# Kernel optimization log

Hardware: AMD Instinct MI355X
Metric: run time of the kernel (lower is better)

## Reference

```python
import jax, jax.numpy as jnp
import numpy as np

B, S, F, U = 64, 512, 128, 512          # seq_length == units (required for broadcast in original code)
SIGDIM = F + F * F                       # level-2 truncated signature dimension
GRID_SIZE, SPLINE_ORDER = 5, 3           # efficient-KAN style defaults
NB = GRID_SIZE + SPLINE_ORDER            # number of b-spline basis functions per input feature
LN_EPS = 1e-3                            # keras LayerNormalization default epsilon


def _make_grid():
    h = 2.0 / GRID_SIZE  # uniform grid on [-1, 1], extended by spline order
    return -1.0 + h * jnp.arange(-SPLINE_ORDER, GRID_SIZE + SPLINE_ORDER + 1, dtype=jnp.float32)


def _b_splines(x, grid):
    # x: (N, F) -> (N, F, NB) via Cox-de Boor recursion
    x = x[..., None]
    bases = ((x >= grid[:-1]) & (x < grid[1:])).astype(x.dtype)
    for p in range(1, SPLINE_ORDER + 1):
        left = (x - grid[:-(p + 1)]) / (grid[p:-1] - grid[:-(p + 1)])
        right = (grid[p + 1:] - x) / (grid[p + 1:] - grid[1:-p])
        bases = left * bases[..., :-1] + right * bases[..., 1:]
    return bases


def _kan_linear(x, base_w, spline_w, grid):
    # KANLinear, no bias / no layernorm: silu base branch + b-spline branch
    lead = x.shape[:-1]
    base = jax.nn.silu(x) @ base_w                                  # (..., U)
    b = _b_splines(x.reshape(-1, x.shape[-1]), grid)                # (N, F, NB)
    spl = jnp.einsum('nfk,ufk->nu', b, spline_w).reshape(*lead, base_w.shape[1])
    return base + spl


def _signature2(x):
    # level-2 path signature of piecewise-linear path x: (B, S, F) -> (B, F + F*F)
    dx = x[:, 1:] - x[:, :-1]                                       # (B, S-1, F)
    s1 = dx.sum(axis=1)                                             # (B, F)
    cs = jnp.cumsum(dx, axis=1)
    prev = jnp.concatenate([jnp.zeros_like(cs[:, :1]), cs[:, :-1]], axis=1)
    s2 = jnp.einsum('bti,btj->bij', prev + 0.5 * dx, dx)            # (B, F, F)
    return jnp.concatenate([s1, s2.reshape(x.shape[0], -1)], axis=-1)


def _grkan(sig, w1, b1, w2, b2, w3, b3, w4, b4, ws, bs, gamma, beta):
    # gated residual network mapping signature -> softmax attention weights (B, U)
    h = jax.nn.elu(sig @ w1 + b1)
    h = h @ w2 + b2
    glu = jax.nn.sigmoid(h @ w3 + b3) * (h @ w4 + b4)
    y = sig @ ws + bs + glu
    mu = jnp.mean(y, axis=-1, keepdims=True)
    var = jnp.var(y, axis=-1, keepdims=True)
    y = (y - mu) / jnp.sqrt(var + LN_EPS) * gamma + beta
    return jax.nn.softmax(y, axis=-1)


def setup_inputs() -> dict:
    key = jax.random.key(0)
    ks = jax.random.split(key, 24)
    n = lambda k, shp, s=0.02: jax.random.normal(k, shp, dtype=jnp.float32) * s
    inp = {
        'inputs': jax.random.normal(ks[0], (B, S, F), dtype=jnp.float32),
        'h_prev': jax.random.normal(ks[1], (B, U), dtype=jnp.float32),
        'c_prev': jax.random.normal(ks[2], (B, U), dtype=jnp.float32),
        'time_kernel': n(ks[3], (S, 1), 0.1),
        'kan_base_w': n(ks[4], (F, U)),
        'kan_spline_w': n(ks[5], (U, F, NB)),
        'g_w1': n(ks[6], (SIGDIM, U)), 'g_b1': jnp.zeros((U,), jnp.float32),
        'g_w2': n(ks[7], (U, U)), 'g_b2': jnp.zeros((U,), jnp.float32),
        'g_w3': n(ks[8], (U, U)), 'g_b3': jnp.zeros((U,), jnp.float32),
        'g_w4': n(ks[9], (U, U)), 'g_b4': jnp.zeros((U,), jnp.float32),
        'g_skip_w': n(ks[10], (SIGDIM, U)), 'g_skip_b': jnp.zeros((U,), jnp.float32),
        'ln_gamma': jnp.ones((U,), jnp.float32), 'ln_beta': jnp.zeros((U,), jnp.float32),
        'wf': n(ks[11], (2 * U, U)), 'bf': jnp.zeros((U,), jnp.float32),
        'wi': n(ks[12], (2 * U, U)), 'bi': jnp.zeros((U,), jnp.float32),
        'wc': n(ks[13], (2 * U, U)), 'bc': jnp.zeros((U,), jnp.float32),
        'wo': n(ks[14], (2 * U, U)), 'bo': jnp.zeros((U,), jnp.float32),
    }
    return inp


def reference(inputs, h_prev, c_prev, time_kernel, kan_base_w, kan_spline_w,
              g_w1, g_b1, g_w2, g_b2, g_w3, g_b3, g_w4, g_b4, g_skip_w, g_skip_b,
              ln_gamma, ln_beta, wf, bf, wi, bi, wc, bc, wo, bo):
    grid = _make_grid()
    weighted = time_kernel * inputs                                  # (B,S,F)
    sig = _signature2(weighted)                                      # (B,SIGDIM)
    attn = _grkan(sig, g_w1, g_b1, g_w2, g_b2, g_w3, g_b3, g_w4, g_b4,
                  g_skip_w, g_skip_b, ln_gamma, ln_beta)             # (B,S) since U==S
    kan_out = _kan_linear(weighted, kan_base_w, kan_spline_w, grid)  # (B,S,U)
    attended = kan_out * attn[..., None]                             # (B,S,U)
    current = attended.mean(axis=1)                                  # (B,U)
    combined = jnp.concatenate([current, h_prev], axis=-1)           # (B,2U)
    f = jax.nn.sigmoid(combined @ wf + bf)
    i = jax.nn.sigmoid(combined @ wi + bi)
    cand = jnp.tanh(combined @ wc + bc)
    o = jax.nn.sigmoid(combined @ wo + bo)
    c_new = f * c_prev + i * cand
    h_new = o * jnp.tanh(c_new)
    return h_new, c_new
```

## Files before the change

### kernel.cpp

```cpp
#include <hip/hip_runtime.h>
#include <math.h>

#define BB 64
#define SS 512
#define FF 128
#define UU 512
#define NBB 8
#define SIGDIM (FF + FF*FF)
#define K3 16512
#define KK 1152
#define SIG_KC 43
#define SIG_STEPS 6

typedef __attribute__((ext_vector_type(8))) __bf16 bf16x8;
typedef __attribute__((ext_vector_type(8))) unsigned short u16x8;
typedef __attribute__((ext_vector_type(4))) float f32x4;

__device__ __forceinline__ unsigned short f2bf(float x) {
    unsigned int u = __float_as_uint(x);
    unsigned int r = u + 0x7FFFu + ((u >> 16) & 1u);
    return (unsigned short)(r >> 16);
}

__device__ __forceinline__ float sigmoidf(float x) { return 1.0f / (1.0f + expf(-x)); }

__global__ void k_wprep(const float* __restrict__ splw, const float* __restrict__ basew,
                        const float* __restrict__ h_prev,
                        unsigned short* __restrict__ Wt, unsigned short* __restrict__ comb_b) {
    int idx = blockIdx.x * 256 + threadIdx.x;
    if (idx >= UU * KK) return;
    int u = idx / KK, c = idx % KK;
    float v = (c < 1024) ? splw[(size_t)u * 1024 + c] : basew[(size_t)(c - 1024) * UU + u];
    Wt[idx] = f2bf(v);
    if (idx < BB * UU) {
        int b = idx >> 9, uu = idx & 511;
        comb_b[(size_t)b * 1024 + 512 + uu] = f2bf(h_prev[idx]);
    }
}

__global__ __launch_bounds__(256) void k_wt3(const float* __restrict__ w2, const float* __restrict__ w3,
                                             const float* __restrict__ w4, const float* __restrict__ wf,
                                             const float* __restrict__ wi, const float* __restrict__ wc,
                                             const float* __restrict__ wo,
                                             unsigned short* __restrict__ W2t,
                                             unsigned short* __restrict__ W3t,
                                             unsigned short* __restrict__ W4t,
                                             unsigned short* __restrict__ Wgt) {
    int kt = blockIdx.x, ut = blockIdx.y, z = blockIdx.z;
    int Kdim = (z < 3) ? 512 : 1024;
    if (kt * 64 >= Kdim) return;
    const float* src;
    unsigned short* dst;
    switch (z) {
        case 0: src = w2; dst = W2t; break;
        case 1: src = w3; dst = W3t; break;
        case 2: src = w4; dst = W4t; break;
        case 3: src = wf; dst = Wgt; break;
        case 4: src = wi; dst = Wgt + (size_t)512 * 1024; break;
        case 5: src = wc; dst = Wgt + (size_t)1024 * 1024; break;
        default: src = wo; dst = Wgt + (size_t)1536 * 1024; break;
    }
    __shared__ float tile[64][67];
    int tid = threadIdx.x;
    int k0 = kt * 64, u0 = ut * 64;
#pragma unroll
    for (int p = 0; p < 4; ++p) {
        int e = p * 256 + tid;
        int kk = e >> 4, c4 = (e & 15) * 4;
        const float4 v = *(const float4*)(src + (size_t)(k0 + kk) * UU + u0 + c4);
        tile[kk][c4 + 0] = v.x;
        tile[kk][c4 + 1] = v.y;
        tile[kk][c4 + 2] = v.z;
        tile[kk][c4 + 3] = v.w;
    }
    __syncthreads();
    int kk0 = (tid & 7) * 8;
#pragma unroll
    for (int p = 0; p < 2; ++p) {
        int uu = (tid >> 3) + p * 32;
        u16x8 ov;
#pragma unroll
        for (int j = 0; j < 8; ++j) ov[j] = f2bf(tile[kk0 + j][uu]);
        *(u16x8*)(dst + (size_t)(u0 + uu) * Kdim + k0 + kk0) = ov;
    }
}

__global__ __launch_bounds__(256) void k_adprep(const float* __restrict__ inp,
                                                const float* __restrict__ tk,
                                                unsigned short* __restrict__ aT,
                                                unsigned short* __restrict__ dT,
                                                unsigned short* __restrict__ wT) {
    int tt0 = blockIdx.x * 64, f0 = blockIdx.y * 64, b = blockIdx.z;
    __shared__ float wS[65][67];
    __shared__ float w0S[64];
    int tid = threadIdx.x;
    const float* ib = inp + (size_t)b * SS * FF;
    if (tid < 64) w0S[tid] = tk[0] * ib[f0 + tid];
#pragma unroll
    for (int p = 0; p < 5; ++p) {
        int e = p * 256 + tid;
        if (e < 65 * 16) {
            int row = e >> 4, c4 = (e & 15) * 4;
            int t = tt0 + row;
            if (t < SS) {
                float tkt = tk[t];
                const float4 v = *(const float4*)(ib + (size_t)t * FF + f0 + c4);
                wS[row][c4 + 0] = tkt * v.x;
                wS[row][c4 + 1] = tkt * v.y;
                wS[row][c4 + 2] = tkt * v.z;
                wS[row][c4 + 3] = tkt * v.w;
            } else {
                wS[row][c4 + 0] = 0.f;
                wS[row][c4 + 1] = 0.f;
                wS[row][c4 + 2] = 0.f;
                wS[row][c4 + 3] = 0.f;
            }
        }
    }
    __syncthreads();
    int t8 = (tid & 7) * 8;
#pragma unroll
    for (int p = 0; p < 2; ++p) {
        int ff = (tid >> 3) + p * 32;
        float w0 = w0S[ff];
        u16x8 av, dv, wv;
#pragma unroll
        for (int j = 0; j < 8; ++j) {
            int tt = t8 + j;
            float w = wS[tt][ff];
            float wn = wS[tt + 1][ff];
            bool valid = (tt0 + tt) < (SS - 1);
            float a = valid ? 0.5f * (w + wn) - w0 : 0.f;
            float d = valid ? wn - w : 0.f;
            av[j] = f2bf(a);
            dv[j] = f2bf(d);
            wv[j] = f2bf(w);
        }
        size_t o = ((size_t)b * FF + f0 + ff) * SS + tt0 + t8;
        *(u16x8*)(aT + o) = av;
        *(u16x8*)(dT + o) = dv;
        *(u16x8*)(wT + o) = wv;
    }
}

__global__ __launch_bounds__(256) void k_sig_mfma(const unsigned short* __restrict__ aT,
                                                  const unsigned short* __restrict__ dT,
                                                  float* __restrict__ s2part) {
    int kc = blockIdx.x, b = blockIdx.y;
    int tid = threadIdx.x, lane = tid & 63;
    int wv = __builtin_amdgcn_readfirstlane(tid >> 6);
    int wrow = (wv & 1) * 64, wcol = (wv >> 1) * 64;
    int k0 = kc * 128;
    const unsigned short* pa = aT + ((size_t)b * FF + wrow + (lane & 15)) * SS + k0 + (lane >> 4) * 8;
    const unsigned short* pd = dT + ((size_t)b * FF + wcol + (lane & 15)) * SS + k0 + (lane >> 4) * 8;
    f32x4 acc[4][4];
#pragma unroll
    for (int i = 0; i < 4; ++i)
#pragma unroll
        for (int j = 0; j < 4; ++j) acc[i][j] = (f32x4)(0.f);
#pragma unroll
    for (int t = 0; t < 4; ++t) {
        bf16x8 af[4], df[4];
#pragma unroll
        for (int rt = 0; rt < 4; ++rt) af[rt] = *(const bf16x8*)(pa + (size_t)rt * 16 * SS + t * 32);
#pragma unroll
        for (int ct = 0; ct < 4; ++ct) df[ct] = *(const bf16x8*)(pd + (size_t)ct * 16 * SS + t * 32);
#pragma unroll
        for (int rt = 0; rt < 4; ++rt)
#pragma unroll
            for (int ct = 0; ct < 4; ++ct)
                acc[rt][ct] = __builtin_amdgcn_mfma_f32_16x16x32_bf16(af[rt], df[ct], acc[rt][ct], 0, 0, 0);
    }
    float* outp = s2part + ((size_t)kc * BB + b) * (FF * FF);
    int quad = lane >> 4, col = lane & 15;
#pragma unroll
    for (int rt = 0; rt < 4; ++rt)
#pragma unroll
        for (int ct = 0; ct < 4; ++ct)
#pragma unroll
            for (int reg = 0; reg < 4; ++reg)
                outp[(wrow + rt * 16 + quad * 4 + reg) * FF + wcol + ct * 16 + col] = acc[rt][ct][reg];
}

__global__ void k_sig_reduce(const float* __restrict__ inp, const float* __restrict__ tk,
                             const float* __restrict__ s2part, unsigned short* __restrict__ sigb) {
    int idx = blockIdx.x * 256 + threadIdx.x;
    if (idx >= BB * SIGDIM) return;
    int b = idx / SIGDIM, r = idx % SIGDIM;
    float v;
    if (r < FF) {
        v = tk[SS - 1] * inp[((size_t)b * SS + SS - 1) * FF + r] - tk[0] * inp[(size_t)b * SS * FF + r];
    } else {
        int ij = r - FF;
        v = 0.f;
#pragma unroll
        for (int c = 0; c < 4; ++c) v += s2part[((size_t)c * BB + b) * (FF * FF) + ij];
    }
    sigb[idx] = f2bf(v);
}

__global__ __launch_bounds__(256) void k_sig_fused(const unsigned short* __restrict__ sigb,
                                                   const float* __restrict__ w1,
                                                   const float* __restrict__ gsw,
                                                   float* __restrict__ spart) {
    int nt = blockIdx.x, kc = blockIdx.y, mat = blockIdx.z;
    const float* src = mat ? gsw : w1;
    __shared__ float tile[64][67];
    int tid = threadIdx.x, lane = tid & 63;
    int wv = __builtin_amdgcn_readfirstlane(tid >> 6);
    int u0 = nt * 64;
    int n0 = wv * 16;
    int kbase = kc * (SIG_STEPS * 64);

    f32x4 acc[4];
#pragma unroll
    for (int i = 0; i < 4; ++i) acc[i] = (f32x4)(0.f);

    int nn = lane & 15;
    int kq = (lane >> 4) * 8;
    const unsigned short* pab = sigb + (size_t)nn * K3 + kq;

    for (int step = 0; step < SIG_STEPS; ++step) {
        int k0 = kbase + step * 64;
#pragma unroll
        for (int p = 0; p < 4; ++p) {
            int e = p * 256 + tid;
            int kk = e >> 4, c4 = (e & 15) * 4;
            const float4 v = *(const float4*)(src + (size_t)(k0 + kk) * UU + u0 + c4);
            tile[kk][c4 + 0] = v.x;
            tile[kk][c4 + 1] = v.y;
            tile[kk][c4 + 2] = v.z;
            tile[kk][c4 + 3] = v.w;
        }
        __syncthreads();
#pragma unroll
        for (int s = 0; s < 2; ++s) {
            u16x8 ub;
            int kb = s * 32 + kq;
#pragma unroll
            for (int j = 0; j < 8; ++j) ub[j] = f2bf(tile[kb + j][n0 + nn]);
            bf16x8 bfrag = __builtin_bit_cast(bf16x8, ub);
#pragma unroll
            for (int rt = 0; rt < 4; ++rt) {
                bf16x8 afrag = *(const bf16x8*)(pab + (size_t)(rt * 16) * K3 + k0 + s * 32);
                acc[rt] = __builtin_amdgcn_mfma_f32_16x16x32_bf16(afrag, bfrag, acc[rt], 0, 0, 0);
            }
        }
        __syncthreads();
    }

    int col = lane & 15, quad = lane >> 4;
    float* P = spart + ((size_t)(mat * SIG_KC + kc) * 64) * UU;
#pragma unroll
    for (int rt = 0; rt < 4; ++rt)
#pragma unroll
        for (int reg = 0; reg < 4; ++reg)
            P[(size_t)(rt * 16 + quad * 4 + reg) * UU + u0 + n0 + col] = acc[rt][reg];
}

__global__ __launch_bounds__(256) void k_sig_red2(const float* __restrict__ spart,
                                                  const float* __restrict__ b1,
                                                  unsigned short* __restrict__ h1b,
                                                  float* __restrict__ skippre) {
    int idx = blockIdx.x * 256 + threadIdx.x;
    int mat = idx >> 15;
    int rem = idx & 32767;
    int m = rem >> 9, n = rem & 511;
    const float* p = spart + ((size_t)(mat * SIG_KC) * 64 + m) * UU + n;
    float v = 0.f;
#pragma unroll
    for (int kc = 0; kc < SIG_KC; ++kc) v += p[(size_t)kc * 64 * UU];
    if (mat == 0) {
        v += b1[n];
        h1b[(size_t)m * UU + n] = f2bf(v > 0.f ? v : expf(v) - 1.0f);
    } else {
        skippre[(size_t)m * UU + n] = v;
    }
}

__global__ __launch_bounds__(64) void k_h2_direct(const unsigned short* __restrict__ h1b,
                                                  const unsigned short* __restrict__ W2t,
                                                  const float* __restrict__ b2,
                                                  unsigned short* __restrict__ h2b) {
    int lane = threadIdx.x;
    int mt = blockIdx.x, nt = blockIdx.y;
    const unsigned short* pa = h1b + (size_t)(mt * 16 + (lane & 15)) * 512 + (lane >> 4) * 8;
    const unsigned short* pb = W2t + (size_t)(nt * 16 + (lane & 15)) * 512 + (lane >> 4) * 8;
    f32x4 acc0 = (f32x4)(0.f), acc1 = (f32x4)(0.f);
#pragma unroll
    for (int t = 0; t < 16; t += 2) {
        bf16x8 a0 = *(const bf16x8*)(pa + t * 32);
        bf16x8 b0 = *(const bf16x8*)(pb + t * 32);
        bf16x8 a1 = *(const bf16x8*)(pa + t * 32 + 32);
        bf16x8 b1v = *(const bf16x8*)(pb + t * 32 + 32);
        acc0 = __builtin_amdgcn_mfma_f32_16x16x32_bf16(a0, b0, acc0, 0, 0, 0);
        acc1 = __builtin_amdgcn_mfma_f32_16x16x32_bf16(a1, b1v, acc1, 0, 0, 0);
    }
    int col = lane & 15, quad = lane >> 4;
    int j = nt * 16 + col;
    float bb = b2[j];
#pragma unroll
    for (int reg = 0; reg < 4; ++reg) {
        int row = mt * 16 + quad * 4 + reg;
        h2b[(size_t)row * UU + j] = f2bf(acc0[reg] + acc1[reg] + bb);
    }
}

__global__ __launch_bounds__(64) void k_glu_direct(const unsigned short* __restrict__ h2b,
                                                   const unsigned short* __restrict__ W3t,
                                                   const unsigned short* __restrict__ W4t,
                                                   const float* __restrict__ b3,
                                                   const float* __restrict__ b4,
                                                   const float* __restrict__ skippre,
                                                   const float* __restrict__ skb,
                                                   float* __restrict__ yv) {
    int lane = threadIdx.x;
    int mt = blockIdx.x, nt = blockIdx.y;
    const unsigned short* pa = h2b + (size_t)(mt * 16 + (lane & 15)) * 512 + (lane >> 4) * 8;
    const unsigned short* pb3 = W3t + (size_t)(nt * 16 + (lane & 15)) * 512 + (lane >> 4) * 8;
    const unsigned short* pb4 = W4t + (size_t)(nt * 16 + (lane & 15)) * 512 + (lane >> 4) * 8;
    f32x4 acc3 = (f32x4)(0.f), acc4 = (f32x4)(0.f);
#pragma unroll
    for (int t = 0; t < 16; ++t) {
        bf16x8 a = *(const bf16x8*)(pa + t * 32);
        bf16x8 b3f = *(const bf16x8*)(pb3 + t * 32);
        bf16x8 b4f = *(const bf16x8*)(pb4 + t * 32);
        acc3 = __builtin_amdgcn_mfma_f32_16x16x32_bf16(a, b3f, acc3, 0, 0, 0);
        acc4 = __builtin_amdgcn_mfma_f32_16x16x32_bf16(a, b4f, acc4, 0, 0, 0);
    }
    int col = lane & 15, quad = lane >> 4;
    int j = nt * 16 + col;
    float bb3 = b3[j], bb4 = b4[j], sb = skb[j];
#pragma unroll
    for (int reg = 0; reg < 4; ++reg) {
        int row = mt * 16 + quad * 4 + reg;
        float g = sigmoidf(acc3[reg] + bb3);
        yv[(size_t)row * UU + j] = skippre[(size_t)row * UU + j] + sb + g * (acc4[reg] + bb4);
    }
}

__device__ __forceinline__ float block_sum(float v, float* red) {
    int tid = threadIdx.x;
#pragma unroll
    for (int off = 32; off > 0; off >>= 1) v += __shfl_down(v, off);
    __syncthreads();
    if ((tid & 63) == 0) red[tid >> 6] = v;
    __syncthreads();
    float r = red[0];
#pragma unroll
    for (int i = 1; i < 8; ++i) r += red[i];
    return r;
}
__device__ __forceinline__ float block_max(float v, float* red) {
    int tid = threadIdx.x;
#pragma unroll
    for (int off = 32; off > 0; off >>= 1) v = fmaxf(v, __shfl_down(v, off));
    __syncthreads();
    if ((tid & 63) == 0) red[tid >> 6] = v;
    __syncthreads();
    float r = red[0];
#pragma unroll
    for (int i = 1; i < 8; ++i) r = fmaxf(r, red[i]);
    return r;
}

__global__ void k_lnsm(const float* __restrict__ yv, const float* __restrict__ gamma,
                       const float* __restrict__ beta, float* __restrict__ attn) {
    int b = blockIdx.x, u = threadIdx.x;
    __shared__ float red[8];
    float v = yv[(size_t)b * UU + u];
    float mu = block_sum(v, red) * (1.0f / UU);
    float d = v - mu;
    float var = block_sum(d * d, red) * (1.0f / UU);
    float z = d * rsqrtf(var + 1e-3f) * gamma[u] + beta[u];
    float m = block_max(z, red);
    float e = expf(z - m);
    float Z = block_sum(e, red);
    attn[(size_t)b * UU + u] = e / Z;
}

__global__ __launch_bounds__(256) void k_kan_red(const unsigned short* __restrict__ wT,
                                                 const float* __restrict__ attn,
                                                 unsigned short* __restrict__ Aredb) {
    int b = blockIdx.x;
    int lane = threadIdx.x & 63;
    int f = blockIdx.y * 4 + (threadIdx.x >> 6);

    const u16x8 wv = *(const u16x8*)(wT + ((size_t)b * FF + f) * SS + lane * 8);
    const float* ap = attn + (size_t)b * UU + lane * 8;
    float4 a0 = *(const float4*)ap;
    float4 a1 = *(const float4*)(ap + 4);

    float acc[9] = {};
#pragma unroll
    for (int s = 0; s < 8; ++s) {
        float w = __uint_as_float((unsigned int)wv[s] << 16);
        float a = (s < 4) ? ((s == 0) ? a0.x : (s == 1) ? a0.y : (s == 2) ? a0.z : a0.w)
                          : ((s == 4) ? a1.x : (s == 5) ? a1.y : (s == 6) ? a1.z : a1.w);
        float t = (w + 2.2f) * 2.5f;
        float cf = floorf(fminf(fmaxf(t, -2.f), 13.f));
        int c = (int)cf;
        float u = t - cf;
        float u2 = u * u, u3 = u2 * u;
        float p0 = u3 * (1.f / 6.f);
        float p1 = (-3.f * u3 + 3.f * u2 + 3.f * u + 1.f) * (1.f / 6.f);
        float p2 = (3.f * u3 - 6.f * u2 + 4.f) * (1.f / 6.f);
        float onemu = 1.f - u;
        float p3 = onemu * onemu * onemu * (1.f / 6.f);
#pragma unroll
        for (int k2 = 0; k2 < 8; ++k2) {
            int d = c - k2;
            float v = (d == 0) ? p0 : (d == 1) ? p1 : (d == 2) ? p2 : (d == 3) ? p3 : 0.f;
            acc[k2] += a * v;
        }
        acc[8] += a * (w * sigmoidf(w));
    }

#pragma unroll
    for (int off = 1; off < 64; off <<= 1) {
#pragma unroll
        for (int k = 0; k < 9; ++k) acc[k] += __shfl_xor(acc[k], off);
    }

    if (lane == 0) {
        const float sc = 1.0f / SS;
        u16x8 ov;
#pragma unroll
        for (int k = 0; k < 8; ++k) ov[k] = f2bf(acc[k] * sc);
        *(u16x8*)(Aredb + (size_t)b * KK + f * 8) = ov;
        Aredb[(size_t)b * KK + 1024 + f] = f2bf(acc[8] * sc);
    }
}

__global__ __launch_bounds__(64) void k_cur_direct(const unsigned short* __restrict__ Aredb,
                                                   const unsigned short* __restrict__ Wt,
                                                   unsigned short* __restrict__ comb_b) {
    int lane = threadIdx.x;
    int mt = blockIdx.x, nt = blockIdx.y;
    const unsigned short* pa = Aredb + (size_t)(mt * 16 + (lane & 15)) * KK + (lane >> 4) * 8;
    const unsigned short* pb = Wt + (size_t)(nt * 16 + (lane & 15)) * KK + (lane >> 4) * 8;
    f32x4 acc0 = (f32x4)(0.f), acc1 = (f32x4)(0.f);
#pragma unroll 6
    for (int t = 0; t < KK / 32; t += 2) {
        bf16x8 a0 = *(const bf16x8*)(pa + t * 32);
        bf16x8 b0 = *(const bf16x8*)(pb + t * 32);
        bf16x8 a1 = *(const bf16x8*)(pa + t * 32 + 32);
        bf16x8 b1v = *(const bf16x8*)(pb + t * 32 + 32);
        acc0 = __builtin_amdgcn_mfma_f32_16x16x32_bf16(a0, b0, acc0, 0, 0, 0);
        acc1 = __builtin_amdgcn_mfma_f32_16x16x32_bf16(a1, b1v, acc1, 0, 0, 0);
    }
    int col = lane & 15, quad = lane >> 4;
    int j = nt * 16 + col;
#pragma unroll
    for (int reg = 0; reg < 4; ++reg) {
        int row = mt * 16 + quad * 4 + reg;
        comb_b[(size_t)row * 1024 + j] = f2bf(acc0[reg] + acc1[reg]);
    }
}

__global__ __launch_bounds__(64) void k_gates_direct(const unsigned short* __restrict__ comb_b,
                                                     const unsigned short* __restrict__ Wgt,
                                                     float* __restrict__ gates) {
    int lane = threadIdx.x;
    int mt = blockIdx.x, nt = blockIdx.y;
    const unsigned short* pa = comb_b + (size_t)(mt * 16 + (lane & 15)) * 1024 + (lane >> 4) * 8;
    const unsigned short* pb = Wgt + (size_t)(nt * 16 + (lane & 15)) * 1024 + (lane >> 4) * 8;
    f32x4 acc0 = (f32x4)(0.f), acc1 = (f32x4)(0.f);
#pragma unroll 8
    for (int t = 0; t < 32; t += 2) {
        bf16x8 a0 = *(const bf16x8*)(pa + t * 32);
        bf16x8 b0 = *(const bf16x8*)(pb + t * 32);
        bf16x8 a1 = *(const bf16x8*)(pa + t * 32 + 32);
        bf16x8 b1v = *(const bf16x8*)(pb + t * 32 + 32);
        acc0 = __builtin_amdgcn_mfma_f32_16x16x32_bf16(a0, b0, acc0, 0, 0, 0);
        acc1 = __builtin_amdgcn_mfma_f32_16x16x32_bf16(a1, b1v, acc1, 0, 0, 0);
    }
    int col = lane & 15, quad = lane >> 4;
    int j = nt * 16 + col;
#pragma unroll
    for (int reg = 0; reg < 4; ++reg) {
        int row = mt * 16 + quad * 4 + reg;
        gates[(size_t)row * 2048 + j] = acc0[reg] + acc1[reg];
    }
}

__global__ void k_cell(const float* __restrict__ gates,
                       const float* __restrict__ bf_, const float* __restrict__ bi_,
                       const float* __restrict__ bc_, const float* __restrict__ bo_,
                       const float* __restrict__ c_prev, float* __restrict__ out) {
    int idx = blockIdx.x * 256 + threadIdx.x;
    if (idx >= BB * UU) return;
    int b = idx >> 9, u = idx & 511;
    const float* g = gates + (size_t)b * 2048;
    float f = sigmoidf(g[u] + bf_[u]);
    float ii = sigmoidf(g[512 + u] + bi_[u]);
    float cd = tanhf(g[1024 + u] + bc_[u]);
    float o = sigmoidf(g[1536 + u] + bo_[u]);
    float cn = f * c_prev[idx] + ii * cd;
    out[idx] = o * tanhf(cn);
    out[(size_t)BB * UU + idx] = cn;
}

extern "C" void kernel_launch(void* const* d_in, const int* in_sizes, int n_in,
                              void* d_out, int out_size, void* d_ws, size_t ws_size,
                              hipStream_t stream) {
    const float* inp   = (const float*)d_in[0];
    const float* hprev = (const float*)d_in[1];
    const float* cprev = (const float*)d_in[2];
    const float* tk    = (const float*)d_in[3];
    const float* basew = (const float*)d_in[4];
    const float* splw  = (const float*)d_in[5];
    const float* gw1   = (const float*)d_in[6];
    const float* gb1   = (const float*)d_in[7];
    const float* gw2   = (const float*)d_in[8];
    const float* gb2   = (const float*)d_in[9];
    const float* gw3   = (const float*)d_in[10];
    const float* gb3   = (const float*)d_in[11];
    const float* gw4   = (const float*)d_in[12];
    const float* gb4   = (const float*)d_in[13];
    const float* gsw   = (const float*)d_in[14];
    const float* gsb   = (const float*)d_in[15];
    const float* lng   = (const float*)d_in[16];
    const float* lnb   = (const float*)d_in[17];
    const float* wf    = (const float*)d_in[18];
    const float* bf_   = (const float*)d_in[19];
    const float* wi    = (const float*)d_in[20];
    const float* bi_   = (const float*)d_in[21];
    const float* wc    = (const float*)d_in[22];
    const float* bc_   = (const float*)d_in[23];
    const float* wo    = (const float*)d_in[24];
    const float* bo_   = (const float*)d_in[25];
    float* out = (float*)d_out;

    float* ws = (float*)d_ws;
    size_t o = 0;
    unsigned short* Wt  = (unsigned short*)(ws + o); o += (size_t)UU * KK / 2;
    float* s2part   = ws + o; o += (size_t)4 * BB * FF * FF;
    unsigned short* aT = (unsigned short*)(ws + o); o += (size_t)BB * FF * SS / 2;
    unsigned short* dT = (unsigned short*)(ws + o); o += (size_t)BB * FF * SS / 2;
    unsigned short* wT = (unsigned short*)(ws + o); o += (size_t)BB * FF * SS / 2;
    unsigned short* sigb = (unsigned short*)(ws + o); o += (size_t)BB * K3 / 2;
    float* spart    = ws + o; o += (size_t)2 * SIG_KC * 64 * UU;
    float* skippre  = ws + o; o += (size_t)BB * UU;
    unsigned short* h1b = (unsigned short*)(ws + o); o += (size_t)BB * UU / 2;
    unsigned short* h2b = (unsigned short*)(ws + o); o += (size_t)BB * UU / 2;
    float* yv       = ws + o; o += (size_t)BB * UU;
    float* attn     = ws + o; o += (size_t)BB * UU;
    unsigned short* Aredb = (unsigned short*)(ws + o); o += (size_t)BB * KK / 2;
    unsigned short* W2t = (unsigned short*)(ws + o); o += (size_t)512 * 512 / 2;
    unsigned short* W3t = (unsigned short*)(ws + o); o += (size_t)512 * 512 / 2;
    unsigned short* W4t = (unsigned short*)(ws + o); o += (size_t)512 * 512 / 2;
    unsigned short* Wgt = (unsigned short*)(ws + o); o += (size_t)2048 * 1024 / 2;
    unsigned short* comb_b = (unsigned short*)(ws + o); o += (size_t)BB * 1024 / 2;
    float* gates    = ws + o; o += (size_t)BB * 2048;
    (void)ws_size; (void)in_sizes; (void)n_in; (void)out_size;

    k_wprep<<<(UU * KK + 255) / 256, 256, 0, stream>>>(splw, basew, hprev, Wt, comb_b);
    k_wt3<<<dim3(16, 8, 7), 256, 0, stream>>>(gw2, gw3, gw4, wf, wi, wc, wo, W2t, W3t, W4t, Wgt);
    k_adprep<<<dim3(8, 2, BB), 256, 0, stream>>>(inp, tk, aT, dT, wT);
    k_sig_mfma<<<dim3(4, BB), 256, 0, stream>>>(aT, dT, s2part);
    k_sig_reduce<<<(BB * SIGDIM + 255) / 256, 256, 0, stream>>>(inp, tk, s2part, sigb);
    k_sig_fused<<<dim3(8, SIG_KC, 2), 256, 0, stream>>>(sigb, gw1, gsw, spart);
    k_sig_red2<<<256, 256, 0, stream>>>(spart, gb1, h1b, skippre);
    k_h2_direct<<<dim3(4, 32), 64, 0, stream>>>(h1b, W2t, gb2, h2b);
    k_glu_direct<<<dim3(4, 32), 64, 0, stream>>>(h2b, W3t, W4t, gb3, gb4, skippre, gsb, yv);
    k_lnsm<<<BB, UU, 0, stream>>>(yv, lng, lnb, attn);
    k_kan_red<<<dim3(BB, FF / 4), 256, 0, stream>>>(wT, attn, Aredb);
    k_cur_direct<<<dim3(4, 32), 64, 0, stream>>>(Aredb, Wt, comb_b);
    k_gates_direct<<<dim3(4, 128), 64, 0, stream>>>(comb_b, Wgt, gates);
    k_cell<<<(BB * UU + 255) / 256, 256, 0, stream>>>(gates, bf_, bi_, bc_, bo_, cprev, out);
}
```

Measured before the change: 252.1 us.

## Merge weight-prep kernels and fuse LSTM gate GEMM with cell update

Combines the two weight-conversion launches into one kernel using a z-slice for the KAN weight/h_prev conversion, which now uses a grid-stride loop. Fuses the gate GEMM with the LSTM cell epilogue: each wave computes all four gate tiles for the same units and applies sigmoid/tanh directly, removing the gates buffer round-trip and one launch. The fused gate kernel launches 128 waves instead of 512, so there is less parallelism. The weight-conversion slice now runs on only 128 blocks looping over the data.

```diff
diff --git a/kernel.cpp b/kernel.cpp
--- a/kernel.cpp
+++ b/kernel.cpp
@@ -5,7 +5,6 @@
 #define SS 512
 #define FF 128
 #define UU 512
-#define NBB 8
 #define SIGDIM (FF + FF*FF)
 #define K3 16512
 #define KK 1152
@@ -24,34 +23,41 @@
 
 __device__ __forceinline__ float sigmoidf(float x) { return 1.0f / (1.0f + expf(-x)); }
 
-__global__ void k_wprep(const float* __restrict__ splw, const float* __restrict__ basew,
-                        const float* __restrict__ h_prev,
-                        unsigned short* __restrict__ Wt, unsigned short* __restrict__ comb_b) {
-    int idx = blockIdx.x * 256 + threadIdx.x;
-    if (idx >= UU * KK) return;
-    int u = idx / KK, c = idx % KK;
-    float v = (c < 1024) ? splw[(size_t)u * 1024 + c] : basew[(size_t)(c - 1024) * UU + u];
-    Wt[idx] = f2bf(v);
-    if (idx < BB * UU) {
-        int b = idx >> 9, uu = idx & 511;
-        comb_b[(size_t)b * 1024 + 512 + uu] = f2bf(h_prev[idx]);
-    }
-}
-
-__global__ __launch_bounds__(256) void k_wt3(const float* __restrict__ w2, const float* __restrict__ w3,
-                                             const float* __restrict__ w4, const float* __restrict__ wf,
-                                             const float* __restrict__ wi, const float* __restrict__ wc,
-                                             const float* __restrict__ wo,
-                                             unsigned short* __restrict__ W2t,
-                                             unsigned short* __restrict__ W3t,
-                                             unsigned short* __restrict__ W4t,
-                                             unsigned short* __restrict__ Wgt) {
-    int kt = blockIdx.x, ut = blockIdx.y, z = blockIdx.z;
-    int Kdim = (z < 3) ? 512 : 1024;
+__global__ __launch_bounds__(256) void k_prep(const float* __restrict__ splw,
+                                              const float* __restrict__ basew,
+                                              const float* __restrict__ h_prev,
+                                              const float* __restrict__ w2, const float* __restrict__ w3,
+                                              const float* __restrict__ w4, const float* __restrict__ wf,
+                                              const float* __restrict__ wi, const float* __restrict__ wc,
+                                              const float* __restrict__ wo,
+                                              unsigned short* __restrict__ Wt,
+                                              unsigned short* __restrict__ comb_b,
+                                              unsigned short* __restrict__ W2t,
+                                              unsigned short* __restrict__ W3t,
+                                              unsigned short* __restrict__ W4t,
+                                              unsigned short* __restrict__ Wgt) {
+    int z = blockIdx.z;
+    int tid = threadIdx.x;
+    if (z == 0) {
+        int base = (blockIdx.y * 16 + blockIdx.x) * 256 + tid;
+        {
+            int b = base >> 9, uu = base & 511;
+            comb_b[(size_t)b * 1024 + 512 + uu] = f2bf(h_prev[base]);
+        }
+        for (int idx = base; idx < UU * KK; idx += 128 * 256) {
+            int u = idx / KK, c = idx % KK;
+            float v = (c < 1024) ? splw[(size_t)u * 1024 + c] : basew[(size_t)(c - 1024) * UU + u];
+            Wt[idx] = f2bf(v);
+        }
+        return;
+    }
+    int zz = z - 1;
+    int Kdim = (zz < 3) ? 512 : 1024;
+    int kt = blockIdx.x, ut = blockIdx.y;
     if (kt * 64 >= Kdim) return;
     const float* src;
     unsigned short* dst;
-    switch (z) {
+    switch (zz) {
         case 0: src = w2; dst = W2t; break;
         case 1: src = w3; dst = W3t; break;
         case 2: src = w4; dst = W4t; break;
@@ -61,7 +67,6 @@
         default: src = wo; dst = Wgt + (size_t)1536 * 1024; break;
     }
     __shared__ float tile[64][67];
-    int tid = threadIdx.x;
     int k0 = kt * 64, u0 = ut * 64;
 #pragma unroll
     for (int p = 0; p < 4; ++p) {
@@ -458,47 +463,48 @@
     }
 }
 
-__global__ __launch_bounds__(64) void k_gates_direct(const unsigned short* __restrict__ comb_b,
-                                                     const unsigned short* __restrict__ Wgt,
-                                                     float* __restrict__ gates) {
+__global__ __launch_bounds__(64) void k_gates_cell(const unsigned short* __restrict__ comb_b,
+                                                   const unsigned short* __restrict__ Wgt,
+                                                   const float* __restrict__ bf_,
+                                                   const float* __restrict__ bi_,
+                                                   const float* __restrict__ bc_,
+                                                   const float* __restrict__ bo_,
+                                                   const float* __restrict__ c_prev,
+                                                   float* __restrict__ out) {
     int lane = threadIdx.x;
-    int mt = blockIdx.x, nt = blockIdx.y;
+    int mt = blockIdx.x, jt = blockIdx.y;
     const unsigned short* pa = comb_b + (size_t)(mt * 16 + (lane & 15)) * 1024 + (lane >> 4) * 8;
-    const unsigned short* pb = Wgt + (size_t)(nt * 16 + (lane & 15)) * 1024 + (lane >> 4) * 8;
-    f32x4 acc0 = (f32x4)(0.f), acc1 = (f32x4)(0.f);
-#pragma unroll 8
-    for (int t = 0; t < 32; t += 2) {
-        bf16x8 a0 = *(const bf16x8*)(pa + t * 32);
-        bf16x8 b0 = *(const bf16x8*)(pb + t * 32);
-        bf16x8 a1 = *(const bf16x8*)(pa + t * 32 + 32);
-        bf16x8 b1v = *(const bf16x8*)(pb + t * 32 + 32);
-        acc0 = __builtin_amdgcn_mfma_f32_16x16x32_bf16(a0, b0, acc0, 0, 0, 0);
-        acc1 = __builtin_amdgcn_mfma_f32_16x16x32_bf16(a1, b1v, acc1, 0, 0, 0);
+    const unsigned short* pb0 = Wgt + (size_t)(0 * 512 + jt * 16 + (lane & 15)) * 1024 + (lane >> 4) * 8;
+    const unsigned short* pb1 = Wgt + (size_t)(1 * 512 + jt * 16 + (lane & 15)) * 1024 + (lane >> 4) * 8;
+    const unsigned short* pb2 = Wgt + (size_t)(2 * 512 + jt * 16 + (lane & 15)) * 1024 + (lane >> 4) * 8;
+    const unsigned short* pb3 = Wgt + (size_t)(3 * 512 + jt * 16 + (lane & 15)) * 1024 + (lane >> 4) * 8;
+    f32x4 accf = (f32x4)(0.f), acci = (f32x4)(0.f), accc = (f32x4)(0.f), acco = (f32x4)(0.f);
+#pragma unroll 4
+    for (int t = 0; t < 32; ++t) {
+        bf16x8 a = *(const bf16x8*)(pa + t * 32);
+        bf16x8 b0 = *(const bf16x8*)(pb0 + t * 32);
+        bf16x8 b1 = *(const bf16x8*)(pb1 + t * 32);
+        bf16x8 b2 = *(const bf16x8*)(pb2 + t * 32);
+        bf16x8 b3 = *(const bf16x8*)(pb3 + t * 32);
+        accf = __builtin_amdgcn_mfma_f32_16x16x32_bf16(a, b0, accf, 0, 0, 0);
+        acci = __builtin_amdgcn_mfma_f32_16x16x32_bf16(a, b1, acci, 0, 0, 0);
+        accc = __builtin_amdgcn_mfma_f32_16x16x32_bf16(a, b2, accc, 0, 0, 0);
+        acco = __builtin_amdgcn_mfma_f32_16x16x32_bf16(a, b3, acco, 0, 0, 0);
     }
     int col = lane & 15, quad = lane >> 4;
-    int j = nt * 16 + col;
+    int j = jt * 16 + col;
+    float bfv = bf_[j], biv = bi_[j], bcv = bc_[j], bov = bo_[j];
 #pragma unroll
     for (int reg = 0; reg < 4; ++reg) {
         int row = mt * 16 + quad * 4 + reg;
-        gates[(size_t)row * 2048 + j] = acc0[reg] + acc1[reg];
-    }
-}
-
-__global__ void k_cell(const float* __restrict__ gates,
-                       const float* __restrict__ bf_, const float* __restrict__ bi_,
-                       const float* __restrict__ bc_, const float* __restrict__ bo_,
-                       const float* __restrict__ c_prev, float* __restrict__ out) {
-    int idx = blockIdx.x * 256 + threadIdx.x;
-    if (idx >= BB * UU) return;
-    int b = idx >> 9, u = idx & 511;
-    const float* g = gates + (size_t)b * 2048;
-    float f = sigmoidf(g[u] + bf_[u]);
-    float ii = sigmoidf(g[512 + u] + bi_[u]);
-    float cd = tanhf(g[1024 + u] + bc_[u]);
-    float o = sigmoidf(g[1536 + u] + bo_[u]);
-    float cn = f * c_prev[idx] + ii * cd;
-    out[idx] = o * tanhf(cn);
-    out[(size_t)BB * UU + idx] = cn;
+        float f = sigmoidf(accf[reg] + bfv);
+        float ii = sigmoidf(acci[reg] + biv);
+        float cd = tanhf(accc[reg] + bcv);
+        float o = sigmoidf(acco[reg] + bov);
+        float cn = f * c_prev[(size_t)row * UU + j] + ii * cd;
+        out[(size_t)row * UU + j] = o * tanhf(cn);
+        out[(size_t)BB * UU + (size_t)row * UU + j] = cn;
+    }
 }
 
 extern "C" void kernel_launch(void* const* d_in, const int* in_sizes, int n_in,
@@ -552,11 +558,10 @@
     unsigned short* W4t = (unsigned short*)(ws + o); o += (size_t)512 * 512 / 2;
     unsigned short* Wgt = (unsigned short*)(ws + o); o += (size_t)2048 * 1024 / 2;
     unsigned short* comb_b = (unsigned short*)(ws + o); o += (size_t)BB * 1024 / 2;
-    float* gates    = ws + o; o += (size_t)BB * 2048;
     (void)ws_size; (void)in_sizes; (void)n_in; (void)out_size;
 
-    k_wprep<<<(UU * KK + 255) / 256, 256, 0, stream>>>(splw, basew, hprev, Wt, comb_b);
-    k_wt3<<<dim3(16, 8, 7), 256, 0, stream>>>(gw2, gw3, gw4, wf, wi, wc, wo, W2t, W3t, W4t, Wgt);
+    k_prep<<<dim3(16, 8, 8), 256, 0, stream>>>(splw, basew, hprev, gw2, gw3, gw4, wf, wi, wc, wo,
+                                               Wt, comb_b, W2t, W3t, W4t, Wgt);
     k_adprep<<<dim3(8, 2, BB), 256, 0, stream>>>(inp, tk, aT, dT, wT);
     k_sig_mfma<<<dim3(4, BB), 256, 0, stream>>>(aT, dT, s2part);
     k_sig_reduce<<<(BB * SIGDIM + 255) / 256, 256, 0, stream>>>(inp, tk, s2part, sigb);
@@ -567,6 +572,5 @@
     k_lnsm<<<BB, UU, 0, stream>>>(yv, lng, lnb, attn);
     k_kan_red<<<dim3(BB, FF / 4), 256, 0, stream>>>(wT, attn, Aredb);
     k_cur_direct<<<dim3(4, 32), 64, 0, stream>>>(Aredb, Wt, comb_b);
-    k_gates_direct<<<dim3(4, 128), 64, 0, stream>>>(comb_b, Wgt, gates);
-    k_cell<<<(BB * UU + 255) / 256, 256, 0, stream>>>(gates, bf_, bi_, bc_, bo_, cprev, out);
-}
+    k_gates_cell<<<dim3(4, 32), 64, 0, stream>>>(comb_b, Wgt, bf_, bi_, bc_, bo_, cprev, out);
+}
```

New measurement: 255.8 us. No clear change (+1.5%).
